# Kernel optimization log

Measured on AMD Instinct MI355X. Metric: run time of the kernel, lower is better.

## Reference

```python
import jax, jax.numpy as jnp
import numpy as np

BN_EPS = 1e-5

def _gcn_conv(x, W, b, src, dst, norm, n_nodes):
    # PyG GCNConv: h = x @ W, then out[dst] += norm_e * h[src] (self-loops included in src/dst), + bias
    h = x @ W                                   # [N, F_out]
    msg = h[src] * norm[:, None]                # [E+N, F_out] gather + scale
    out = jax.ops.segment_sum(msg, dst, num_segments=n_nodes)
    return out + b

def _batchnorm(x, gamma, beta):
    # training-mode BN over node axis (biased variance, as torch normalizes with)
    mu = jnp.mean(x, axis=0)
    var = jnp.mean((x - mu) ** 2, axis=0)
    return gamma * (x - mu) * jax.lax.rsqrt(var + BN_EPS) + beta

def setup_inputs() -> dict:
    key = jax.random.key(0)
    ks = jax.random.split(key, 8)
    N, E, Din, H = 100000, 1600000, 128, 128
    x = jax.random.normal(ks[0], (N, Din), dtype=jnp.float32)
    edge_index = jax.random.randint(ks[1], (2, E), 0, N, dtype=jnp.int64)
    def glorot(k, shape):
        lim = float(np.sqrt(6.0 / (shape[0] + shape[1])))
        return jax.random.uniform(k, shape, jnp.float32, -lim, lim)
    return {
        "x": x, "edge_index": edge_index,
        "W1": glorot(ks[2], (Din, H)), "b1": jnp.zeros((H,), jnp.float32),
        "g1": jnp.ones((H,), jnp.float32), "be1": jnp.zeros((H,), jnp.float32),
        "W2": glorot(ks[3], (H, H // 2)), "b2": jnp.zeros((H // 2,), jnp.float32),
        "g2": jnp.ones((H // 2,), jnp.float32), "be2": jnp.zeros((H // 2,), jnp.float32),
        "Wf": glorot(ks[4], (H // 2, 2)), "bf": jnp.zeros((2,), jnp.float32),
    }

def reference(x, edge_index, W1, b1, g1, be1, W2, b2, g2, be2, Wf, bf):
    N = x.shape[0]
    loops = jnp.arange(N, dtype=edge_index.dtype)
    src = jnp.concatenate([edge_index[0], loops])   # add self-loops
    dst = jnp.concatenate([edge_index[1], loops])
    # symmetric GCN normalization: deg from A + I (unit edge weights)
    deg = jax.ops.segment_sum(jnp.ones_like(dst, dtype=x.dtype), dst, num_segments=N)
    dinv = jax.lax.rsqrt(deg)                       # deg >= 1 thanks to self-loops
    norm = dinv[src] * dinv[dst]                    # [E+N]

    h = _gcn_conv(x, W1, b1, src, dst, norm, N)
    h = jax.nn.relu(_batchnorm(h, g1, be1))
    h = _gcn_conv(h, W2, b2, src, dst, norm, N)
    h = jax.nn.relu(_batchnorm(h, g2, be2))
    return h @ Wf + bf                              # [N, 2] logits
```

## Files before the change

### kernel.cpp

```cpp
#include <hip/hip_runtime.h>
#include <hip/hip_fp16.h>
#include <cstdint>
#include <cstddef>

#define BN_EPS 1e-5f
#define NBLK 256

typedef _Float16 f16x8 __attribute__((ext_vector_type(8)));
typedef float f32x4 __attribute__((ext_vector_type(4)));

__global__ __launch_bounds__(256) void k_flag(const int* __restrict__ e, int* __restrict__ flag, int nSamples,
                                              float* __restrict__ stats1, float* __restrict__ stats2) {
    __shared__ int acc;
    if (threadIdx.x == 0) acc = 0;
    __syncthreads();
    int v = 0;
    for (int i = threadIdx.x; i < nSamples; i += 256) v |= e[2 * i + 1];
    atomicOr(&acc, v);
    if (threadIdx.x < 256) stats1[threadIdx.x] = 0.0f;
    if (threadIdx.x < 128) stats2[threadIdx.x] = 0.0f;
    __syncthreads();
    if (threadIdx.x == 0) *flag = (acc == 0) ? 1 : 0;
}

__device__ __forceinline__ int ld_src(const int* e, int E, int i, int is64) {
    return is64 ? e[2 * i] : e[i];
}
__device__ __forceinline__ int ld_dst(const int* e, int E, int i, int is64) {
    return is64 ? e[2 * (E + i)] : e[E + i];
}

__global__ __launch_bounds__(256) void k_bcount(const int* __restrict__ e, const int* __restrict__ flag,
                                                int* __restrict__ cntMat, int E, int nbC) {
    __shared__ int c[512];
    const int t = threadIdx.x, blk = blockIdx.x;
    for (int b = t; b < nbC; b += 256) c[b] = 0;
    __syncthreads();
    const int is64 = *flag;
    const int chunk = (E + NBLK - 1) / NBLK;
    const int e0 = blk * chunk;
    const int e1 = min(E, e0 + chunk);
    for (int i = e0 + t; i < e1; i += 256) {
        int d = ld_dst(e, E, i, is64);
        atomicAdd(&c[d >> 9], 1);
    }
    __syncthreads();
    for (int b = t; b < nbC; b += 256) cntMat[b * NBLK + blk] = c[b];
}

__global__ __launch_bounds__(256) void k_scan1(const int* __restrict__ in, int* __restrict__ outp,
                                               int* __restrict__ blockSums, int M) {
    __shared__ int sh[256];
    const int t = threadIdx.x;
    const int base = blockIdx.x * 1024 + t * 4;
    int v[4];
#pragma unroll
    for (int i = 0; i < 4; ++i) v[i] = (base + i < M) ? in[base + i] : 0;
    int tot = v[0] + v[1] + v[2] + v[3];
    sh[t] = tot;
    __syncthreads();
    int val = tot;
    for (int o = 1; o < 256; o <<= 1) {
        int x = (t >= o) ? sh[t - o] : 0;
        __syncthreads();
        val += x;
        sh[t] = val;
        __syncthreads();
    }
    int run = val - tot;
#pragma unroll
    for (int i = 0; i < 4; ++i) {
        if (base + i < M) outp[base + i] = run;
        run += v[i];
    }
    if (t == 255) blockSums[blockIdx.x] = val;
}

__global__ __launch_bounds__(256) void k_scan2(int* __restrict__ blockSums, int nB) {
    __shared__ int sh[256];
    const int t = threadIdx.x;
    const int base = t * 4;
    int v[4];
#pragma unroll
    for (int i = 0; i < 4; ++i) v[i] = (base + i < nB) ? blockSums[base + i] : 0;
    int tot = v[0] + v[1] + v[2] + v[3];
    sh[t] = tot;
    __syncthreads();
    int val = tot;
    for (int o = 1; o < 256; o <<= 1) {
        int x = (t >= o) ? sh[t - o] : 0;
        __syncthreads();
        val += x;
        sh[t] = val;
        __syncthreads();
    }
    int run = val - tot;
#pragma unroll
    for (int i = 0; i < 4; ++i) {
        if (base + i < nB) blockSums[base + i] = run;
        run += v[i];
    }
}

__global__ __launch_bounds__(256) void k_scan3(int* __restrict__ outp, const int* __restrict__ blockSums, int M) {
    const int t = threadIdx.x;
    const int off = blockSums[blockIdx.x];
    const int base = blockIdx.x * 1024 + t * 4;
#pragma unroll
    for (int i = 0; i < 4; ++i) {
        int idx = base + i;
        if (idx < M) outp[idx] += off;
    }
}

__global__ __launch_bounds__(256) void k_bscatter(const int* __restrict__ e, const int* __restrict__ flag,
                                                  const int* __restrict__ ofsMat, unsigned* __restrict__ pairBuf,
                                                  int E, int nbC) {
    __shared__ int ofs[512];
    const int t = threadIdx.x, blk = blockIdx.x;
    for (int b = t; b < nbC; b += 256) ofs[b] = ofsMat[b * NBLK + blk];
    __syncthreads();
    const int is64 = *flag;
    const int chunk = (E + NBLK - 1) / NBLK;
    const int e0 = blk * chunk;
    const int e1 = min(E, e0 + chunk);
    for (int i = e0 + t; i < e1; i += 256) {
        int s = ld_src(e, E, i, is64);
        int d = ld_dst(e, E, i, is64);
        int pos = atomicAdd(&ofs[d >> 9], 1);
        pairBuf[pos] = ((unsigned)(d & 511) << 23) | (unsigned)s;
    }
}

__global__ __launch_bounds__(256) void k_fsort(const unsigned* __restrict__ pairBuf, const int* __restrict__ ofsMat,
                                               int* __restrict__ csrSrc, int* __restrict__ rowPtr,
                                               int* __restrict__ cnt, float* __restrict__ dinv,
                                               int E, int N, int nbC) {
    __shared__ int hist[512];
    __shared__ int lofs[512];
    __shared__ int sc[256];
    const int t = threadIdx.x, b = blockIdx.x;
    const int lo = ofsMat[b * NBLK];
    const int hi = (b + 1 < nbC) ? ofsMat[(b + 1) * NBLK] : E;
    hist[t] = 0; hist[t + 256] = 0;
    __syncthreads();
    for (int i = lo + t; i < hi; i += 256) atomicAdd(&hist[pairBuf[i] >> 23], 1);
    __syncthreads();
    int v0 = hist[2 * t], v1 = hist[2 * t + 1];
    int tot = v0 + v1;
    sc[t] = tot;
    __syncthreads();
    int val = tot;
    for (int o = 1; o < 256; o <<= 1) {
        int x = (t >= o) ? sc[t - o] : 0;
        __syncthreads();
        val += x;
        sc[t] = val;
        __syncthreads();
    }
    int excl = val - tot;
    const int d0 = b * 512 + 2 * t;
    const int d1 = d0 + 1;
    lofs[2 * t] = lo + excl;
    lofs[2 * t + 1] = lo + excl + v0;
    if (d0 < N) { rowPtr[d0] = lo + excl;      cnt[d0] = v0; dinv[d0] = rsqrtf((float)(v0 + 1)); }
    if (d1 < N) { rowPtr[d1] = lo + excl + v0; cnt[d1] = v1; dinv[d1] = rsqrtf((float)(v1 + 1)); }
    __syncthreads();
    for (int i = lo + t; i < hi; i += 256) {
        unsigned p = pairBuf[i];
        int dL = p >> 23;
        int s = (int)(p & 0x7FFFFFu);
        int pos = atomicAdd(&lofs[dL], 1);
        csrSrc[pos] = s;
    }
}

__global__ __launch_bounds__(256, 2) void k_gemm1(const float* __restrict__ x, const float* __restrict__ W,
                                                  const float* __restrict__ dinv,
                                                  _Float16* __restrict__ hs1, int N) {
    __shared__ _Float16 Ws[128][136];
    __shared__ _Float16 xs[128][136];
    const int t = threadIdx.x;
    const int row0 = blockIdx.x * 128;

#pragma unroll
    for (int i = 0; i < 16; ++i) {
        int j = t + i * 256;
        int k = j >> 5, c = (j & 31) << 2;
        float4 v = ((const float4*)W)[j];
        union { _Float16 h[4]; uint2 u; } p;
        p.h[0] = (_Float16)v.x; p.h[1] = (_Float16)v.y; p.h[2] = (_Float16)v.z; p.h[3] = (_Float16)v.w;
        *(uint2*)&Ws[k][c] = p.u;
    }
#pragma unroll
    for (int i = 0; i < 16; ++i) {
        int j = t + i * 256;
        int r = j >> 5, c = (j & 31) << 2;
        int gr = row0 + r;
        float4 v = make_float4(0.f, 0.f, 0.f, 0.f);
        if (gr < N) v = *(const float4*)&x[(size_t)gr * 128 + c];
        union { _Float16 h[4]; uint2 u; } p;
        p.h[0] = (_Float16)v.x; p.h[1] = (_Float16)v.y; p.h[2] = (_Float16)v.z; p.h[3] = (_Float16)v.w;
        *(uint2*)&xs[r][c] = p.u;
    }
    __syncthreads();

    const int w = t >> 6, l = t & 63;
    const int wm = w >> 1, wn = w & 1;
    const int l15 = l & 15, lg = l >> 4;

    f16x8 bfr[4][4];
#pragma unroll
    for (int nt = 0; nt < 4; ++nt)
#pragma unroll
        for (int ks = 0; ks < 4; ++ks) {
            int col = wn * 64 + nt * 16 + l15;
            int kb = ks * 32 + lg * 8;
            f16x8 b;
#pragma unroll
            for (int j = 0; j < 8; ++j) b[j] = Ws[kb + j][col];
            bfr[nt][ks] = b;
        }

    f32x4 acc[4][4];
#pragma unroll
    for (int mt = 0; mt < 4; ++mt)
#pragma unroll
        for (int nt = 0; nt < 4; ++nt) acc[mt][nt] = (f32x4)(0.f);

#pragma unroll
    for (int mt = 0; mt < 4; ++mt) {
        const int r = wm * 64 + mt * 16 + l15;
        f16x8 afr[4];
#pragma unroll
        for (int ks = 0; ks < 4; ++ks) afr[ks] = *(const f16x8*)&xs[r][ks * 32 + lg * 8];
#pragma unroll
        for (int nt = 0; nt < 4; ++nt)
#pragma unroll
            for (int ks = 0; ks < 4; ++ks)
                acc[mt][nt] = __builtin_amdgcn_mfma_f32_16x16x32_f16(afr[ks], bfr[nt][ks], acc[mt][nt], 0, 0, 0);
    }

#pragma unroll
    for (int mt = 0; mt < 4; ++mt) {
        const int rbase = row0 + wm * 64 + mt * 16 + lg * 4;
#pragma unroll
        for (int rr = 0; rr < 4; ++rr) {
            int gr = rbase + rr;
            if (gr < N) {
                float dv = dinv[gr];
#pragma unroll
                for (int nt = 0; nt < 4; ++nt) {
                    int col = wn * 64 + nt * 16 + l15;
                    hs1[(size_t)gr * 128 + col] = (_Float16)(acc[mt][nt][rr] * dv);
                }
            }
        }
    }
}

__global__ __launch_bounds__(256) void k_gather128(const int* __restrict__ csrSrc, const int* __restrict__ rowPtr,
                                                   const int* __restrict__ cnt, const float* __restrict__ dinv,
                                                   const __half2* __restrict__ hs, __half2* __restrict__ agg, int N) {
    int wv = (blockIdx.x * 256 + threadIdx.x) >> 6;
    if (wv >= N) return;
    const int d = __builtin_amdgcn_readfirstlane(wv);
    const int lane = threadIdx.x & 63;
    const size_t fo = (size_t)d * 64 + lane;
    float2 acc = __half22float2(hs[fo]);
    const int start = __builtin_amdgcn_readfirstlane(rowPtr[d]);
    const int c = __builtin_amdgcn_readfirstlane(cnt[d]);
    const int* __restrict__ p = csrSrc + start;
    int j = 0;
    for (; j + 7 < c; j += 8) {
        float2 v[8];
#pragma unroll
        for (int u = 0; u < 8; ++u) v[u] = __half22float2(hs[(size_t)p[j + u] * 64 + lane]);
#pragma unroll
        for (int u = 0; u < 8; ++u) { acc.x += v[u].x; acc.y += v[u].y; }
    }
    for (; j + 3 < c; j += 4) {
        float2 v[4];
#pragma unroll
        for (int u = 0; u < 4; ++u) v[u] = __half22float2(hs[(size_t)p[j + u] * 64 + lane]);
#pragma unroll
        for (int u = 0; u < 4; ++u) { acc.x += v[u].x; acc.y += v[u].y; }
    }
    for (; j < c; ++j) {
        float2 v = __half22float2(hs[(size_t)p[j] * 64 + lane]);
        acc.x += v.x; acc.y += v.y;
    }
    const float wgt = dinv[d];
    agg[fo] = __floats2half2_rn(acc.x * wgt, acc.y * wgt);
}

__global__ __launch_bounds__(256) void k_gather64(const int* __restrict__ csrSrc, const int* __restrict__ rowPtr,
                                                  const int* __restrict__ cnt, const float* __restrict__ dinv,
                                                  const __half* __restrict__ hs, __half* __restrict__ agg, int N) {
    int wv = (blockIdx.x * 256 + threadIdx.x) >> 6;
    if (wv >= N) return;
    const int d = __builtin_amdgcn_readfirstlane(wv);
    const int lane = threadIdx.x & 63;
    const size_t fo = (size_t)d * 64 + lane;
    float acc = __half2float(hs[fo]);
    const int start = __builtin_amdgcn_readfirstlane(rowPtr[d]);
    const int c = __builtin_amdgcn_readfirstlane(cnt[d]);
    const int* __restrict__ p = csrSrc + start;
    int j = 0;
    for (; j + 7 < c; j += 8) {
        float v[8];
#pragma unroll
        for (int u = 0; u < 8; ++u) v[u] = __half2float(hs[(size_t)p[j + u] * 64 + lane]);
#pragma unroll
        for (int u = 0; u < 8; ++u) acc += v[u];
    }
    for (; j + 3 < c; j += 4) {
        float v[4];
#pragma unroll
        for (int u = 0; u < 4; ++u) v[u] = __half2float(hs[(size_t)p[j + u] * 64 + lane]);
#pragma unroll
        for (int u = 0; u < 4; ++u) acc += v[u];
    }
    for (; j < c; ++j) acc += __half2float(hs[(size_t)p[j] * 64 + lane]);
    agg[fo] = __float2half(acc * dinv[d]);
}

template <int F>
__global__ __launch_bounds__(256) void k_stats_h(const __half2* __restrict__ a, float* __restrict__ stats, int N) {
    const int S = F / 2;
    const int t = threadIdx.x;
    const int slot = t & (S - 1);
    const int sub = t / S;
    const int rpb = 256 / S;
    float sx = 0.f, sy = 0.f, qx = 0.f, qy = 0.f;
    for (int r = blockIdx.x * rpb + sub; r < N; r += gridDim.x * rpb) {
        float2 v = __half22float2(a[(size_t)r * S + slot]);
        sx += v.x; sy += v.y;
        qx += v.x * v.x; qy += v.y * v.y;
    }
    __shared__ float l0[256], l1[256], l2[256], l3[256];
    l0[t] = sx; l1[t] = sy; l2[t] = qx; l3[t] = qy;
    __syncthreads();
    if (t < S) {
#pragma unroll
        for (int i = 1; i < rpb; ++i) {
            sx += l0[t + i * S]; sy += l1[t + i * S];
            qx += l2[t + i * S]; qy += l3[t + i * S];
        }
        atomicAdd(&stats[2 * t], sx);
        atomicAdd(&stats[2 * t + 1], sy);
        atomicAdd(&stats[F + 2 * t], qx);
        atomicAdd(&stats[F + 2 * t + 1], qy);
    }
}

__global__ void k_bnparam(const float* __restrict__ stats, const float* __restrict__ g, const float* __restrict__ be,
                          float* __restrict__ ss, int N, int F) {
    int f = threadIdx.x;
    if (f < F) {
        float invN = 1.0f / (float)N;
        float mean = stats[f] * invN;
        float var = stats[F + f] * invN - mean * mean;
        var = fmaxf(var, 0.f);
        float inv = rsqrtf(var + BN_EPS);
        float scale = g[f] * inv;
        ss[f] = scale;
        ss[F + f] = be[f] - mean * scale;
    }
}

__global__ __launch_bounds__(256, 2) void k_gemm2(const __half* __restrict__ a_in, const float* __restrict__ W,
                                                  const float* __restrict__ ss, const float* __restrict__ dinv,
                                                  _Float16* __restrict__ hs2, int N) {
    __shared__ _Float16 Ws[128][72];
    __shared__ _Float16 xs[128][136];
    const int t = threadIdx.x;
    const int row0 = blockIdx.x * 128;

#pragma unroll
    for (int i = 0; i < 8; ++i) {
        int j = t + i * 256;
        int k = j >> 4, c = (j & 15) << 2;
        float4 v = ((const float4*)W)[j];
        union { _Float16 h[4]; uint2 u; } p;
        p.h[0] = (_Float16)v.x; p.h[1] = (_Float16)v.y; p.h[2] = (_Float16)v.z; p.h[3] = (_Float16)v.w;
        *(uint2*)&Ws[k][c] = p.u;
    }
#pragma unroll
    for (int i = 0; i < 16; ++i) {
        int j = t + i * 256;
        int r = j >> 5, c = (j & 31) << 2;
        int gr = row0 + r;
        float4 v = make_float4(0.f, 0.f, 0.f, 0.f);
        if (gr < N) {
            union { uint2 u; __half2 h[2]; } iv;
            iv.u = *(const uint2*)&a_in[(size_t)gr * 128 + c];
            float2 v01 = __half22float2(iv.h[0]);
            float2 v23 = __half22float2(iv.h[1]);
            float4 sc = *(const float4*)&ss[c];
            float4 sh = *(const float4*)&ss[128 + c];
            v.x = fmaxf(0.f, fmaf(v01.x, sc.x, sh.x));
            v.y = fmaxf(0.f, fmaf(v01.y, sc.y, sh.y));
            v.z = fmaxf(0.f, fmaf(v23.x, sc.z, sh.z));
            v.w = fmaxf(0.f, fmaf(v23.y, sc.w, sh.w));
        }
        union { _Float16 h[4]; uint2 u; } p;
        p.h[0] = (_Float16)v.x; p.h[1] = (_Float16)v.y; p.h[2] = (_Float16)v.z; p.h[3] = (_Float16)v.w;
        *(uint2*)&xs[r][c] = p.u;
    }
    __syncthreads();

    const int w = t >> 6, l = t & 63;
    const int wm = w >> 1, wn = w & 1;
    const int l15 = l & 15, lg = l >> 4;

    f16x8 bfr[2][4];
#pragma unroll
    for (int nt = 0; nt < 2; ++nt)
#pragma unroll
        for (int ks = 0; ks < 4; ++ks) {
            int col = wn * 32 + nt * 16 + l15;
            int kb = ks * 32 + lg * 8;
            f16x8 b;
#pragma unroll
            for (int j = 0; j < 8; ++j) b[j] = Ws[kb + j][col];
            bfr[nt][ks] = b;
        }

    f32x4 acc[4][2];
#pragma unroll
    for (int mt = 0; mt < 4; ++mt)
#pragma unroll
        for (int nt = 0; nt < 2; ++nt) acc[mt][nt] = (f32x4)(0.f);

#pragma unroll
    for (int mt = 0; mt < 4; ++mt) {
        const int r = wm * 64 + mt * 16 + l15;
        f16x8 afr[4];
#pragma unroll
        for (int ks = 0; ks < 4; ++ks) afr[ks] = *(const f16x8*)&xs[r][ks * 32 + lg * 8];
#pragma unroll
        for (int nt = 0; nt < 2; ++nt)
#pragma unroll
            for (int ks = 0; ks < 4; ++ks)
                acc[mt][nt] = __builtin_amdgcn_mfma_f32_16x16x32_f16(afr[ks], bfr[nt][ks], acc[mt][nt], 0, 0, 0);
    }

#pragma unroll
    for (int mt = 0; mt < 4; ++mt) {
        const int rbase = row0 + wm * 64 + mt * 16 + lg * 4;
#pragma unroll
        for (int rr = 0; rr < 4; ++rr) {
            int gr = rbase + rr;
            if (gr < N) {
                float dv = dinv[gr];
#pragma unroll
                for (int nt = 0; nt < 2; ++nt) {
                    int col = wn * 32 + nt * 16 + l15;
                    hs2[(size_t)gr * 64 + col] = (_Float16)(acc[mt][nt][rr] * dv);
                }
            }
        }
    }
}

__global__ __launch_bounds__(256) void k_final(const __half* __restrict__ a_in, const float* __restrict__ ss,
                                               const float* __restrict__ Wf, const float* __restrict__ bf,
                                               float* __restrict__ out, int N) {
    __shared__ float buf[256][65];
    const int t = threadIdx.x;
    const int row0 = blockIdx.x * 256;

#pragma unroll
    for (int i = 0; i < 16; ++i) {
        int j = t + i * 256;
        int r = j >> 4;
        int k = (j & 15) << 2;
        float4 v = make_float4(0.f, 0.f, 0.f, 0.f);
        int gr = row0 + r;
        if (gr < N) {
            union { uint2 u; __half2 h[2]; } iv;
            iv.u = *(const uint2*)&a_in[(size_t)gr * 64 + k];
            float2 v01 = __half22float2(iv.h[0]);
            float2 v23 = __half22float2(iv.h[1]);
            float4 sc = *(const float4*)&ss[k];
            float4 sh = *(const float4*)&ss[64 + k];
            v.x = fmaxf(0.f, fmaf(v01.x, sc.x, sh.x));
            v.y = fmaxf(0.f, fmaf(v01.y, sc.y, sh.y));
            v.z = fmaxf(0.f, fmaf(v23.x, sc.z, sh.z));
            v.w = fmaxf(0.f, fmaf(v23.y, sc.w, sh.w));
        }
        buf[r][k + 0] = v.x; buf[r][k + 1] = v.y; buf[r][k + 2] = v.z; buf[r][k + 3] = v.w;
    }
    __syncthreads();

    int gr = row0 + t;
    if (gr < N) {
        float a0 = 0.f, a1 = 0.f;
        for (int k = 0; k < 64; ++k) {
            float v = buf[t][k];
            a0 = fmaf(v, Wf[2 * k + 0], a0);
            a1 = fmaf(v, Wf[2 * k + 1], a1);
        }
        out[(size_t)gr * 2 + 0] = a0 + bf[0];
        out[(size_t)gr * 2 + 1] = a1 + bf[1];
    }
}

extern "C" void kernel_launch(void* const* d_in, const int* in_sizes, int n_in,
                              void* d_out, int out_size, void* d_ws, size_t ws_size,
                              hipStream_t stream) {
    const float* x   = (const float*)d_in[0];
    const int*   ei  = (const int*)d_in[1];
    const float* W1  = (const float*)d_in[2];
    const float* g1  = (const float*)d_in[4];
    const float* be1 = (const float*)d_in[5];
    const float* W2  = (const float*)d_in[6];
    const float* g2  = (const float*)d_in[8];
    const float* be2 = (const float*)d_in[9];
    const float* Wf  = (const float*)d_in[10];
    const float* bf  = (const float*)d_in[11];
    float* out = (float*)d_out;

    const int N = in_sizes[0] / 128;
    const int E = in_sizes[1] / 2;
    const int nbC = (N + 511) >> 9;
    const int M = nbC * NBLK;
    const int nBs = (M + 1023) / 1024;

    float* fws = (float*)d_ws;
    int*   flag   = (int*)fws;
    float* stats1 = fws + 64;
    float* stats2 = fws + 320;
    float* ss1    = fws + 448;
    float* ss2    = fws + 704;
    int*   blockSums = (int*)(fws + 832);

    const size_t Na = (size_t)((N + 255) & ~255);
    const size_t Ea = (size_t)((E + 255) & ~255);
    const size_t Ma = (size_t)((M + 255) & ~255);
    size_t off = 2048;
    int*   cnt    = (int*)(fws + off);  off += Na;
    int*   rowPtr = (int*)(fws + off);  off += Na;
    float* dinv   = fws + off;          off += Na;
    int*   cntMat = (int*)(fws + off);  off += Ma;
    int*   ofsMat = (int*)(fws + off);  off += Ma;
    int*   csrSrc = (int*)(fws + off);  off += Ea;
    _Float16* hs1 = (_Float16*)(fws + off);
    __half*  agg1 = (__half*)(fws + off + (size_t)N * 64);
    _Float16* hs2 = hs1;
    __half*  agg2 = agg1;
    unsigned* pairBuf = (unsigned*)hs1;

    int nSamp = E < 65536 ? E : 65536;

    k_flag<<<1, 256, 0, stream>>>(ei, flag, nSamp, stats1, stats2);

    k_bcount<<<NBLK, 256, 0, stream>>>(ei, flag, cntMat, E, nbC);
    k_scan1<<<nBs, 256, 0, stream>>>(cntMat, ofsMat, blockSums, M);
    k_scan2<<<1, 256, 0, stream>>>(blockSums, nBs);
    k_scan3<<<nBs, 256, 0, stream>>>(ofsMat, blockSums, M);
    k_bscatter<<<NBLK, 256, 0, stream>>>(ei, flag, ofsMat, pairBuf, E, nbC);
    k_fsort<<<nbC, 256, 0, stream>>>(pairBuf, ofsMat, csrSrc, rowPtr, cnt, dinv, E, N, nbC);

    k_gemm1<<<(N + 127) / 128, 256, 0, stream>>>(x, W1, dinv, hs1, N);
    k_gather128<<<(N * 64 + 255) / 256, 256, 0, stream>>>(csrSrc, rowPtr, cnt, dinv,
                                                          (const __half2*)hs1, (__half2*)agg1, N);
    k_stats_h<128><<<512, 256, 0, stream>>>((const __half2*)agg1, stats1, N);
    k_bnparam<<<1, 128, 0, stream>>>(stats1, g1, be1, ss1, N, 128);

    k_gemm2<<<(N + 127) / 128, 256, 0, stream>>>(agg1, W2, ss1, dinv, hs2, N);
    k_gather64<<<(N * 64 + 255) / 256, 256, 0, stream>>>(csrSrc, rowPtr, cnt, dinv,
                                                         (const __half*)hs2, agg2, N);
    k_stats_h<64><<<512, 256, 0, stream>>>((const __half2*)agg2, stats2, N);
    k_bnparam<<<1, 128, 0, stream>>>(stats2, g2, be2, ss2, N, 64);

    k_final<<<(N + 255) / 256, 256, 0, stream>>>(agg2, ss2, Wf, bf, out, N);
}
```

Measured before the change: 325.1 us.

## Vectorize neighbor gathers with 16-byte loads and cross-lane edge-parallel reduction

Result: faster. 297.3 us (-8.6%).

```diff
diff --git a/kernel.cpp b/kernel.cpp
--- a/kernel.cpp
+++ b/kernel.cpp
@@ -265,64 +265,136 @@
     int wv = (blockIdx.x * 256 + threadIdx.x) >> 6;
     if (wv >= N) return;
     const int d = __builtin_amdgcn_readfirstlane(wv);
-    const int lane = threadIdx.x & 63;
-    const size_t fo = (size_t)d * 64 + lane;
-    float2 acc = __half22float2(hs[fo]);
+    const int l = threadIdx.x & 63;
+    const int q = l >> 4, f = l & 15;
+
+    float2 acc[4];
+    if (q == 0) {
+        union { uint4 u; __half2 h[4]; } v;
+        v.u = *(const uint4*)&hs[(size_t)d * 64 + f * 4];
+#pragma unroll
+        for (int i = 0; i < 4; ++i) acc[i] = __half22float2(v.h[i]);
+    } else {
+#pragma unroll
+        for (int i = 0; i < 4; ++i) acc[i] = make_float2(0.f, 0.f);
+    }
+
     const int start = __builtin_amdgcn_readfirstlane(rowPtr[d]);
     const int c = __builtin_amdgcn_readfirstlane(cnt[d]);
     const int* __restrict__ p = csrSrc + start;
     int j = 0;
     for (; j + 7 < c; j += 8) {
-        float2 v[8];
-#pragma unroll
-        for (int u = 0; u < 8; ++u) v[u] = __half22float2(hs[(size_t)p[j + u] * 64 + lane]);
-#pragma unroll
-        for (int u = 0; u < 8; ++u) { acc.x += v[u].x; acc.y += v[u].y; }
-    }
-    for (; j + 3 < c; j += 4) {
-        float2 v[4];
-#pragma unroll
-        for (int u = 0; u < 4; ++u) v[u] = __half22float2(hs[(size_t)p[j + u] * 64 + lane]);
-#pragma unroll
-        for (int u = 0; u < 4; ++u) { acc.x += v[u].x; acc.y += v[u].y; }
-    }
-    for (; j < c; ++j) {
-        float2 v = __half22float2(hs[(size_t)p[j] * 64 + lane]);
-        acc.x += v.x; acc.y += v.y;
-    }
-    const float wgt = dinv[d];
-    agg[fo] = __floats2half2_rn(acc.x * wgt, acc.y * wgt);
+        int s0 = p[j + q], s1 = p[j + 4 + q];
+        union { uint4 u; __half2 h[4]; } v0, v1;
+        v0.u = *(const uint4*)&hs[(size_t)s0 * 64 + f * 4];
+        v1.u = *(const uint4*)&hs[(size_t)s1 * 64 + f * 4];
+#pragma unroll
+        for (int i = 0; i < 4; ++i) {
+            float2 a = __half22float2(v0.h[i]);
+            float2 b = __half22float2(v1.h[i]);
+            acc[i].x += a.x + b.x;
+            acc[i].y += a.y + b.y;
+        }
+    }
+    for (; j < c; j += 4) {
+        int idx = j + q;
+        if (idx < c) {
+            union { uint4 u; __half2 h[4]; } v;
+            v.u = *(const uint4*)&hs[(size_t)p[idx] * 64 + f * 4];
+#pragma unroll
+            for (int i = 0; i < 4; ++i) {
+                float2 a = __half22float2(v.h[i]);
+                acc[i].x += a.x;
+                acc[i].y += a.y;
+            }
+        }
+    }
+
+#pragma unroll
+    for (int i = 0; i < 4; ++i) {
+        acc[i].x += __shfl_xor(acc[i].x, 16);
+        acc[i].y += __shfl_xor(acc[i].y, 16);
+        acc[i].x += __shfl_xor(acc[i].x, 32);
+        acc[i].y += __shfl_xor(acc[i].y, 32);
+    }
+
+    if (q == 0) {
+        const float wgt = dinv[d];
+        union { uint4 u; __half2 h[4]; } o;
+#pragma unroll
+        for (int i = 0; i < 4; ++i) o.h[i] = __floats2half2_rn(acc[i].x * wgt, acc[i].y * wgt);
+        *(uint4*)&agg[(size_t)d * 64 + f * 4] = o.u;
+    }
 }
 
 __global__ __launch_bounds__(256) void k_gather64(const int* __restrict__ csrSrc, const int* __restrict__ rowPtr,
                                                   const int* __restrict__ cnt, const float* __restrict__ dinv,
-                                                  const __half* __restrict__ hs, __half* __restrict__ agg, int N) {
+                                                  const __half2* __restrict__ hs, __half2* __restrict__ agg, int N) {
     int wv = (blockIdx.x * 256 + threadIdx.x) >> 6;
     if (wv >= N) return;
     const int d = __builtin_amdgcn_readfirstlane(wv);
-    const int lane = threadIdx.x & 63;
-    const size_t fo = (size_t)d * 64 + lane;
-    float acc = __half2float(hs[fo]);
+    const int l = threadIdx.x & 63;
+    const int g = l >> 3, f = l & 7;
+
+    float2 acc[4];
+    if (g == 0) {
+        union { uint4 u; __half2 h[4]; } v;
+        v.u = *(const uint4*)&hs[(size_t)d * 32 + f * 4];
+#pragma unroll
+        for (int i = 0; i < 4; ++i) acc[i] = __half22float2(v.h[i]);
+    } else {
+#pragma unroll
+        for (int i = 0; i < 4; ++i) acc[i] = make_float2(0.f, 0.f);
+    }
+
     const int start = __builtin_amdgcn_readfirstlane(rowPtr[d]);
     const int c = __builtin_amdgcn_readfirstlane(cnt[d]);
     const int* __restrict__ p = csrSrc + start;
     int j = 0;
-    for (; j + 7 < c; j += 8) {
-        float v[8];
-#pragma unroll
-        for (int u = 0; u < 8; ++u) v[u] = __half2float(hs[(size_t)p[j + u] * 64 + lane]);
-#pragma unroll
-        for (int u = 0; u < 8; ++u) acc += v[u];
-    }
-    for (; j + 3 < c; j += 4) {
-        float v[4];
-#pragma unroll
-        for (int u = 0; u < 4; ++u) v[u] = __half2float(hs[(size_t)p[j + u] * 64 + lane]);
-#pragma unroll
-        for (int u = 0; u < 4; ++u) acc += v[u];
-    }
-    for (; j < c; ++j) acc += __half2float(hs[(size_t)p[j] * 64 + lane]);
-    agg[fo] = __float2half(acc * dinv[d]);
+    for (; j + 15 < c; j += 16) {
+        int s0 = p[j + g], s1 = p[j + 8 + g];
+        union { uint4 u; __half2 h[4]; } v0, v1;
+        v0.u = *(const uint4*)&hs[(size_t)s0 * 32 + f * 4];
+        v1.u = *(const uint4*)&hs[(size_t)s1 * 32 + f * 4];
+#pragma unroll
+        for (int i = 0; i < 4; ++i) {
+            float2 a = __half22float2(v0.h[i]);
+            float2 b = __half22float2(v1.h[i]);
+            acc[i].x += a.x + b.x;
+            acc[i].y += a.y + b.y;
+        }
+    }
+    for (; j < c; j += 8) {
+        int idx = j + g;
+        if (idx < c) {
+            union { uint4 u; __half2 h[4]; } v;
+            v.u = *(const uint4*)&hs[(size_t)p[idx] * 32 + f * 4];
+#pragma unroll
+            for (int i = 0; i < 4; ++i) {
+                float2 a = __half22float2(v.h[i]);
+                acc[i].x += a.x;
+                acc[i].y += a.y;
+            }
+        }
+    }
+
+#pragma unroll
+    for (int i = 0; i < 4; ++i) {
+        acc[i].x += __shfl_xor(acc[i].x, 8);
+        acc[i].y += __shfl_xor(acc[i].y, 8);
+        acc[i].x += __shfl_xor(acc[i].x, 16);
+        acc[i].y += __shfl_xor(acc[i].y, 16);
+        acc[i].x += __shfl_xor(acc[i].x, 32);
+        acc[i].y += __shfl_xor(acc[i].y, 32);
+    }
+
+    if (g == 0) {
+        const float wgt = dinv[d];
+        union { uint4 u; __half2 h[4]; } o;
+#pragma unroll
+        for (int i = 0; i < 4; ++i) o.h[i] = __floats2half2_rn(acc[i].x * wgt, acc[i].y * wgt);
+        *(uint4*)&agg[(size_t)d * 32 + f * 4] = o.u;
+    }
 }
 
 template <int F>
@@ -552,7 +624,7 @@
     __half*  agg2 = agg1;
     unsigned* pairBuf = (unsigned*)hs1;
 
-    int nSamp = E < 65536 ? E : 65536;
+    int nSamp = E < 2048 ? E : 2048;
 
     k_flag<<<1, 256, 0, stream>>>(ei, flag, nSamp, stats1, stats2);
 
@@ -571,7 +643,7 @@
 
     k_gemm2<<<(N + 127) / 128, 256, 0, stream>>>(agg1, W2, ss1, dinv, hs2, N);
     k_gather64<<<(N * 64 + 255) / 256, 256, 0, stream>>>(csrSrc, rowPtr, cnt, dinv,
-                                                         (const __half*)hs2, agg2, N);
+                                                         (const __half2*)hs2, (__half2*)agg2, N);
     k_stats_h<64><<<512, 256, 0, stream>>>((const __half2*)agg2, stats2, N);
     k_bnparam<<<1, 128, 0, stream>>>(stats2, g2, be2, ss2, N, 64);
 
```

## Fold scan fixup into consumers, widen gathers, shrink dtype-detection sample

Applied to the files above, without the earlier changes.

Result: faster. 308.2 us (-5.2%).

```diff
diff --git a/kernel.cpp b/kernel.cpp
--- a/kernel.cpp
+++ b/kernel.cpp
@@ -102,23 +102,15 @@
     }
 }
 
-__global__ __launch_bounds__(256) void k_scan3(int* __restrict__ outp, const int* __restrict__ blockSums, int M) {
-    const int t = threadIdx.x;
-    const int off = blockSums[blockIdx.x];
-    const int base = blockIdx.x * 1024 + t * 4;
-#pragma unroll
-    for (int i = 0; i < 4; ++i) {
-        int idx = base + i;
-        if (idx < M) outp[idx] += off;
-    }
-}
-
 __global__ __launch_bounds__(256) void k_bscatter(const int* __restrict__ e, const int* __restrict__ flag,
-                                                  const int* __restrict__ ofsMat, unsigned* __restrict__ pairBuf,
-                                                  int E, int nbC) {
+                                                  const int* __restrict__ ofsMat, const int* __restrict__ blockSums,
+                                                  unsigned* __restrict__ pairBuf, int E, int nbC) {
     __shared__ int ofs[512];
     const int t = threadIdx.x, blk = blockIdx.x;
-    for (int b = t; b < nbC; b += 256) ofs[b] = ofsMat[b * NBLK + blk];
+    for (int b = t; b < nbC; b += 256) {
+        int idx = b * NBLK + blk;
+        ofs[b] = ofsMat[idx] + blockSums[idx >> 10];
+    }
     __syncthreads();
     const int is64 = *flag;
     const int chunk = (E + NBLK - 1) / NBLK;
@@ -133,6 +125,7 @@
 }
 
 __global__ __launch_bounds__(256) void k_fsort(const unsigned* __restrict__ pairBuf, const int* __restrict__ ofsMat,
+                                               const int* __restrict__ blockSums,
                                                int* __restrict__ csrSrc, int* __restrict__ rowPtr,
                                                int* __restrict__ cnt, float* __restrict__ dinv,
                                                int E, int N, int nbC) {
@@ -140,8 +133,13 @@
     __shared__ int lofs[512];
     __shared__ int sc[256];
     const int t = threadIdx.x, b = blockIdx.x;
-    const int lo = ofsMat[b * NBLK];
-    const int hi = (b + 1 < nbC) ? ofsMat[(b + 1) * NBLK] : E;
+    const int i0 = b * NBLK;
+    const int lo = ofsMat[i0] + blockSums[i0 >> 10];
+    int hi = E;
+    if (b + 1 < nbC) {
+        const int i1 = (b + 1) * NBLK;
+        hi = ofsMat[i1] + blockSums[i1 >> 10];
+    }
     hist[t] = 0; hist[t + 256] = 0;
     __syncthreads();
     for (int i = lo + t; i < hi; i += 256) atomicAdd(&hist[pairBuf[i] >> 23], 1);
@@ -272,6 +270,16 @@
     const int c = __builtin_amdgcn_readfirstlane(cnt[d]);
     const int* __restrict__ p = csrSrc + start;
     int j = 0;
+    for (; j + 15 < c; j += 16) {
+        int s[16];
+#pragma unroll
+        for (int u = 0; u < 16; ++u) s[u] = p[j + u];
+        float2 v[16];
+#pragma unroll
+        for (int u = 0; u < 16; ++u) v[u] = __half22float2(hs[(size_t)s[u] * 64 + lane]);
+#pragma unroll
+        for (int u = 0; u < 16; ++u) { acc.x += v[u].x; acc.y += v[u].y; }
+    }
     for (; j + 7 < c; j += 8) {
         float2 v[8];
 #pragma unroll
@@ -296,33 +304,47 @@
 
 __global__ __launch_bounds__(256) void k_gather64(const int* __restrict__ csrSrc, const int* __restrict__ rowPtr,
                                                   const int* __restrict__ cnt, const float* __restrict__ dinv,
-                                                  const __half* __restrict__ hs, __half* __restrict__ agg, int N) {
+                                                  const __half2* __restrict__ hs, __half2* __restrict__ agg, int N) {
     int wv = (blockIdx.x * 256 + threadIdx.x) >> 6;
     if (wv >= N) return;
     const int d = __builtin_amdgcn_readfirstlane(wv);
-    const int lane = threadIdx.x & 63;
-    const size_t fo = (size_t)d * 64 + lane;
-    float acc = __half2float(hs[fo]);
+    const int l = threadIdx.x & 63;
+    const int g = l >> 5, f = l & 31;
+
+    float2 acc;
+    if (g == 0) acc = __half22float2(hs[(size_t)d * 32 + f]);
+    else        acc = make_float2(0.f, 0.f);
+
     const int start = __builtin_amdgcn_readfirstlane(rowPtr[d]);
     const int c = __builtin_amdgcn_readfirstlane(cnt[d]);
     const int* __restrict__ p = csrSrc + start;
     int j = 0;
-    for (; j + 7 < c; j += 8) {
-        float v[8];
-#pragma unroll
-        for (int u = 0; u < 8; ++u) v[u] = __half2float(hs[(size_t)p[j + u] * 64 + lane]);
-#pragma unroll
-        for (int u = 0; u < 8; ++u) acc += v[u];
-    }
-    for (; j + 3 < c; j += 4) {
-        float v[4];
-#pragma unroll
-        for (int u = 0; u < 4; ++u) v[u] = __half2float(hs[(size_t)p[j + u] * 64 + lane]);
-#pragma unroll
-        for (int u = 0; u < 4; ++u) acc += v[u];
-    }
-    for (; j < c; ++j) acc += __half2float(hs[(size_t)p[j] * 64 + lane]);
-    agg[fo] = __float2half(acc * dinv[d]);
+    for (; j + 15 < c; j += 16) {
+        int s[8];
+#pragma unroll
+        for (int u = 0; u < 8; ++u) s[u] = p[j + 2 * u + g];
+        float2 v[8];
+#pragma unroll
+        for (int u = 0; u < 8; ++u) v[u] = __half22float2(hs[(size_t)s[u] * 32 + f]);
+#pragma unroll
+        for (int u = 0; u < 8; ++u) { acc.x += v[u].x; acc.y += v[u].y; }
+    }
+    for (; j + 1 < c; j += 2) {
+        float2 v = __half22float2(hs[(size_t)p[j + g] * 32 + f]);
+        acc.x += v.x; acc.y += v.y;
+    }
+    if (j < c && g == 0) {
+        float2 v = __half22float2(hs[(size_t)p[j] * 32 + f]);
+        acc.x += v.x; acc.y += v.y;
+    }
+
+    acc.x += __shfl_xor(acc.x, 32);
+    acc.y += __shfl_xor(acc.y, 32);
+
+    if (g == 0) {
+        const float wgt = dinv[d];
+        agg[(size_t)d * 32 + f] = __floats2half2_rn(acc.x * wgt, acc.y * wgt);
+    }
 }
 
 template <int F>
@@ -552,16 +574,15 @@
     __half*  agg2 = agg1;
     unsigned* pairBuf = (unsigned*)hs1;
 
-    int nSamp = E < 65536 ? E : 65536;
+    int nSamp = E < 2048 ? E : 2048;
 
     k_flag<<<1, 256, 0, stream>>>(ei, flag, nSamp, stats1, stats2);
 
     k_bcount<<<NBLK, 256, 0, stream>>>(ei, flag, cntMat, E, nbC);
     k_scan1<<<nBs, 256, 0, stream>>>(cntMat, ofsMat, blockSums, M);
     k_scan2<<<1, 256, 0, stream>>>(blockSums, nBs);
-    k_scan3<<<nBs, 256, 0, stream>>>(ofsMat, blockSums, M);
-    k_bscatter<<<NBLK, 256, 0, stream>>>(ei, flag, ofsMat, pairBuf, E, nbC);
-    k_fsort<<<nbC, 256, 0, stream>>>(pairBuf, ofsMat, csrSrc, rowPtr, cnt, dinv, E, N, nbC);
+    k_bscatter<<<NBLK, 256, 0, stream>>>(ei, flag, ofsMat, blockSums, pairBuf, E, nbC);
+    k_fsort<<<nbC, 256, 0, stream>>>(pairBuf, ofsMat, blockSums, csrSrc, rowPtr, cnt, dinv, E, N, nbC);
 
     k_gemm1<<<(N + 127) / 128, 256, 0, stream>>>(x, W1, dinv, hs1, N);
     k_gather128<<<(N * 64 + 255) / 256, 256, 0, stream>>>(csrSrc, rowPtr, cnt, dinv,
@@ -571,7 +592,7 @@
 
     k_gemm2<<<(N + 127) / 128, 256, 0, stream>>>(agg1, W2, ss1, dinv, hs2, N);
     k_gather64<<<(N * 64 + 255) / 256, 256, 0, stream>>>(csrSrc, rowPtr, cnt, dinv,
-                                                         (const __half*)hs2, agg2, N);
+                                                         (const __half2*)hs2, (__half2*)agg2, N);
     k_stats_h<64><<<512, 256, 0, stream>>>((const __half2*)agg2, stats2, N);
     k_bnparam<<<1, 128, 0, stream>>>(stats2, g2, be2, ss2, N, 64);
 
```
